# Performance work log

Hardware: AMD Instinct MI355X
Metric: run time of the kernel (lower is better)

Reference implementation:

```python
import jax, jax.numpy as jnp
import numpy as np

B, S, D, H = 16, 577, 1408, 16
HD = D // H  # 88


def setup_inputs() -> dict:
    key = jax.random.key(0)
    k1, k2, k3, k4, k5, k6 = jax.random.split(key, 6)
    hidden_states = jax.random.normal(k1, (B, S, D), dtype=jnp.float32)
    # realistic rotary table: cos/sin pairs stacked in last dim
    theta = jax.random.normal(k2, (S, HD // 2), dtype=jnp.float32)
    freqs_ci = jnp.stack([jnp.cos(theta), jnp.sin(theta)], axis=-1)  # (S, HD/2, 2)
    wqkv = jax.random.normal(k3, (3 * D, D), dtype=jnp.float32) * 0.02
    bqkv = jax.random.normal(k4, (3 * D,), dtype=jnp.float32) * 0.02
    wo = jax.random.normal(k5, (D, D), dtype=jnp.float32) * 0.02
    bo = jax.random.normal(k6, (D,), dtype=jnp.float32) * 0.02
    return {"hidden_states": hidden_states, "freqs_ci": freqs_ci,
            "wqkv": wqkv, "bqkv": bqkv, "wo": wo, "bo": bo}


def reference(hidden_states, freqs_ci, wqkv, bqkv, wo, bo):
    b, s, d = hidden_states.shape
    # fused QKV projection (torch Linear: x @ W.T + b)
    qkv = hidden_states @ wqkv.T + bqkv  # (B, S, 3D)
    q, k, v = jnp.split(qkv, 3, axis=-1)
    q = q.reshape(b, s, H, HD)
    k = k.reshape(b, s, H, HD)
    v = v.reshape(b, s, H, HD)

    cos = freqs_ci[..., 0][None, :, None, :]  # (1, S, 1, HD/2)
    sin = freqs_ci[..., 1][None, :, None, :]

    def rot(x):
        xr = x.reshape(b, s, H, HD // 2, 2)
        xe, xo = xr[..., 0], xr[..., 1]
        re = xe * cos - xo * sin
        ro = xe * sin + xo * cos
        return jnp.stack([re, ro], axis=-1).reshape(b, s, H, HD)

    q = rot(q)
    k = rot(k)

    scale = 1.0 / jnp.sqrt(jnp.float32(HD))  # SDPA default scaling
    scores = jnp.einsum('bqhd,bkhd->bhqk', q, k) * scale
    attn = jax.nn.softmax(scores, axis=-1)
    ctx = jnp.einsum('bhqk,bkhd->bqhd', attn, v).reshape(b, s, d)
    return ctx @ wo.T + bo
```

## Files before the change

kernel.cpp:

```cpp
#include <hip/hip_runtime.h>

typedef __attribute__((ext_vector_type(8))) __bf16 bf16x8;
typedef __attribute__((ext_vector_type(4))) float f32x4;
typedef __attribute__((ext_vector_type(4))) unsigned int uint4v;

#define B_ 16
#define S_ 577
#define D_ 1408
#define H_ 16
#define HD_ 88
#define MROWS (B_*S_)
#define N1 (3*D_)
#define K_ D_
#define KSTEPS 44
#define VT_LD 592
#define SCALE 0.10660035817780521f

static __device__ __forceinline__ void async16(void* lds, const void* g) {
  __builtin_amdgcn_global_load_lds((const __attribute__((address_space(1))) void*)g,
                                   (__attribute__((address_space(3))) void*)lds, 16, 0, 0);
}

static __device__ __forceinline__ int xcd_swizzle(int orig, int nwg) {
  int xcd = orig & 7, lid = orig >> 3;
  int q = nwg >> 3, r = nwg & 7;
  return (xcd < r ? xcd * (q + 1) : r * (q + 1) + (xcd - r) * q) + lid;
}

__global__ void cast_bf16_kernel(const float* __restrict__ src, __bf16* __restrict__ dst, int n4) {
  int i = blockIdx.x * blockDim.x + threadIdx.x;
  if (i >= n4) return;
  const float4 v = ((const float4*)src)[i];
  __bf16* d = dst + (size_t)i * 4;
  d[0] = (__bf16)v.x; d[1] = (__bf16)v.y; d[2] = (__bf16)v.z; d[3] = (__bf16)v.w;
}

__launch_bounds__(256, 2)
__global__ void gemm_qkv_rope(const __bf16* __restrict__ A, const __bf16* __restrict__ Bm,
                              const float* __restrict__ bias, const float* __restrict__ freqs,
                              __bf16* __restrict__ Qb, __bf16* __restrict__ Kb,
                              __bf16* __restrict__ Vb) {
  __shared__ __bf16 As[2][128 * 32];
  __shared__ __bf16 Bs[2][128 * 32];
  const int tid = threadIdx.x;
  const int w = tid >> 6, l = tid & 63;
  const int wgid = xcd_swizzle(blockIdx.x, 33 * 73);
  const int m0 = (wgid % 73) * 128, n0 = (wgid / 73) * 128;
  const int wr = w & 1, wc = w >> 1;
  const int M = MROWS, K = K_;

  f32x4 acc[4][4];
#pragma unroll
  for (int m = 0; m < 4; ++m)
#pragma unroll
    for (int n = 0; n < 4; ++n) acc[m][n] = (f32x4){0.f, 0.f, 0.f, 0.f};

  int arow0 = m0 + w * 32 + (l >> 2);      if (arow0 >= M) arow0 = M - 1;
  int arow1 = m0 + w * 32 + 16 + (l >> 2); if (arow1 >= M) arow1 = M - 1;
  const __bf16* ag0 = A + (size_t)arow0 * K + (l & 3) * 8;
  const __bf16* ag1 = A + (size_t)arow1 * K + (l & 3) * 8;
  const __bf16* bg0 = Bm + (size_t)(n0 + w * 32 + (l >> 2)) * K + (l & 3) * 8;
  const __bf16* bg1 = Bm + (size_t)(n0 + w * 32 + 16 + (l >> 2)) * K + (l & 3) * 8;

  auto stage = [&](int buf, int k0) {
    async16(&As[buf][(w * 32) * 32],      ag0 + k0);
    async16(&As[buf][(w * 32 + 16) * 32], ag1 + k0);
    async16(&Bs[buf][(w * 32) * 32],      bg0 + k0);
    async16(&Bs[buf][(w * 32 + 16) * 32], bg1 + k0);
  };

  stage(0, 0);
  __syncthreads();
  for (int t = 0; t < KSTEPS; ++t) {
    const int cur = t & 1;
    if (t < KSTEPS - 1) stage(cur ^ 1, (t + 1) * 32);
    bf16x8 a[4], b[4];
#pragma unroll
    for (int m = 0; m < 4; ++m)
      a[m] = *(const bf16x8*)&As[cur][(wr * 64 + m * 16 + (l & 15)) * 32 + (l >> 4) * 8];
#pragma unroll
    for (int n = 0; n < 4; ++n)
      b[n] = *(const bf16x8*)&Bs[cur][(wc * 64 + n * 16 + (l & 15)) * 32 + (l >> 4) * 8];
#pragma unroll
    for (int m = 0; m < 4; ++m)
#pragma unroll
      for (int n = 0; n < 4; ++n)
        acc[m][n] = __builtin_amdgcn_mfma_f32_16x16x32_bf16(a[m], b[n], acc[m][n], 0, 0, 0);
    __syncthreads();
  }

  const int sect = n0 / 1408;
  __bf16* dst = (sect == 0) ? Qb : (sect == 1 ? Kb : Vb);
#pragma unroll
  for (int n = 0; n < 4; ++n) {
    const int col = n0 + wc * 64 + n * 16 + (l & 15);
    const int cin = col - sect * 1408;
    const int h = cin / 88, d = cin % 88;
    const float bv = bias[col];
    const int i2 = d & ~1;
    const float sgn = (d & 1) ? 1.f : -1.f;
#pragma unroll
    for (int m = 0; m < 4; ++m) {
      const int rbase = m0 + wr * 64 + m * 16 + (l >> 4) * 4;
#pragma unroll
      for (int j = 0; j < 4; ++j) {
        const int r = rbase + j;
        float val = acc[m][n][j] + bv;
        const int s = r % 577;
        float outv;
        if (sect < 2) {
          const float2 cs = *(const float2*)&freqs[s * 88 + i2];
          const float p = __shfl_xor(val, 1);
          outv = val * cs.x + sgn * p * cs.y;
        } else {
          outv = val;
        }
        if (r < M) {
          const int b = r / 577;
          dst[((size_t)(b * 16 + h) * 577 + s) * 88 + d] = (__bf16)outv;
        }
      }
    }
  }
}

__launch_bounds__(256, 2)
__global__ void gemm_out_bias(const __bf16* __restrict__ A, const __bf16* __restrict__ Bm,
                              const float* __restrict__ bias, float* __restrict__ C) {
  __shared__ __bf16 As[2][128 * 32];
  __shared__ __bf16 Bs[2][128 * 32];
  const int tid = threadIdx.x;
  const int w = tid >> 6, l = tid & 63;
  const int wgid = xcd_swizzle(blockIdx.x, 11 * 73);
  const int m0 = (wgid % 73) * 128, n0 = (wgid / 73) * 128;
  const int wr = w & 1, wc = w >> 1;
  const int M = MROWS, N = D_, K = K_;

  f32x4 acc[4][4];
#pragma unroll
  for (int m = 0; m < 4; ++m)
#pragma unroll
    for (int n = 0; n < 4; ++n) acc[m][n] = (f32x4){0.f, 0.f, 0.f, 0.f};

  int arow0 = m0 + w * 32 + (l >> 2);      if (arow0 >= M) arow0 = M - 1;
  int arow1 = m0 + w * 32 + 16 + (l >> 2); if (arow1 >= M) arow1 = M - 1;
  const __bf16* ag0 = A + (size_t)arow0 * K + (l & 3) * 8;
  const __bf16* ag1 = A + (size_t)arow1 * K + (l & 3) * 8;
  const __bf16* bg0 = Bm + (size_t)(n0 + w * 32 + (l >> 2)) * K + (l & 3) * 8;
  const __bf16* bg1 = Bm + (size_t)(n0 + w * 32 + 16 + (l >> 2)) * K + (l & 3) * 8;

  auto stage = [&](int buf, int k0) {
    async16(&As[buf][(w * 32) * 32],      ag0 + k0);
    async16(&As[buf][(w * 32 + 16) * 32], ag1 + k0);
    async16(&Bs[buf][(w * 32) * 32],      bg0 + k0);
    async16(&Bs[buf][(w * 32 + 16) * 32], bg1 + k0);
  };

  stage(0, 0);
  __syncthreads();
  for (int t = 0; t < KSTEPS; ++t) {
    const int cur = t & 1;
    if (t < KSTEPS - 1) stage(cur ^ 1, (t + 1) * 32);
    bf16x8 a[4], b[4];
#pragma unroll
    for (int m = 0; m < 4; ++m)
      a[m] = *(const bf16x8*)&As[cur][(wr * 64 + m * 16 + (l & 15)) * 32 + (l >> 4) * 8];
#pragma unroll
    for (int n = 0; n < 4; ++n)
      b[n] = *(const bf16x8*)&Bs[cur][(wc * 64 + n * 16 + (l & 15)) * 32 + (l >> 4) * 8];
#pragma unroll
    for (int m = 0; m < 4; ++m)
#pragma unroll
      for (int n = 0; n < 4; ++n)
        acc[m][n] = __builtin_amdgcn_mfma_f32_16x16x32_bf16(a[m], b[n], acc[m][n], 0, 0, 0);
    __syncthreads();
  }

#pragma unroll
  for (int n = 0; n < 4; ++n) {
    int col = n0 + wc * 64 + n * 16 + (l & 15);
    float bv = bias[col];
#pragma unroll
    for (int m = 0; m < 4; ++m) {
      int rbase = m0 + wr * 64 + m * 16 + (l >> 4) * 4;
#pragma unroll
      for (int j = 0; j < 4; ++j) {
        int r = rbase + j;
        if (r < M) C[(size_t)r * N + col] = acc[m][n][j] + bv;
      }
    }
  }
}

__global__ void transpose_v(const __bf16* __restrict__ V, __bf16* __restrict__ Vt_g) {
  __shared__ __bf16 Ls[64 * 104];
  const int bh = blockIdx.x, t = blockIdx.y, s0 = t * 64;
  const int tid = threadIdx.x;
  const __bf16* vp = V + (size_t)bh * 577 * 88;
  for (int i = tid; i < 64 * 11; i += 256) {
    int r = i / 11, off = i % 11;
    int gs = s0 + r; if (gs > 576) gs = 576;
    *(uint4v*)&Ls[r * 104 + off * 8] = *(const uint4v*)(vp + (size_t)gs * 88 + off * 8);
  }
  __syncthreads();
  for (int i = tid; i < 88 * 8; i += 256) {
    int d = i / 8, so = (i % 8) * 8;
    int sc_ = s0 + so;
    if (sc_ < VT_LD) {
      __bf16 tmp[8];
#pragma unroll
      for (int j = 0; j < 8; ++j) tmp[j] = Ls[(so + j) * 104 + d];
      *(uint4v*)&Vt_g[((size_t)bh * 88 + d) * VT_LD + sc_] = *(uint4v*)tmp;
    }
  }
}

__launch_bounds__(256, 3)
__global__ void attn_kernel(const __bf16* __restrict__ Q, const __bf16* __restrict__ K,
                            const __bf16* __restrict__ Vt_gp, __bf16* __restrict__ ctx) {
  __shared__ __bf16 lds[26368];
  const int tid = threadIdx.x;
  const int w = tid >> 6, l = tid & 63;
  const int bh = blockIdx.x;
  const int q0 = blockIdx.y * 128;
  const __bf16* qp = Q + (size_t)bh * 577 * 88;
  const __bf16* kp = K + (size_t)bh * 577 * 88;
  const __bf16* vtp = Vt_gp + (size_t)bh * 88 * VT_LD;
  __bf16* Qs = lds;
  __bf16* Ks = lds + 12288;
  __bf16* Vt = lds + 17920;
  __bf16* Pw = lds + w * 2304;

  for (int i = tid; i < 128 * 11; i += 256) {
    int r = i / 11, off = i % 11;
    int gr = q0 + r; if (gr > 576) gr = 576;
    *(uint4v*)&Qs[r * 96 + off * 8] = *(const uint4v*)(qp + (size_t)gr * 88 + off * 8);
  }
  if (tid < 128) { uint4v z = 0; *(uint4v*)&Qs[tid * 96 + 88] = z; }
  __syncthreads();

  bf16x8 qf[2][3];
#pragma unroll
  for (int mg = 0; mg < 2; ++mg)
#pragma unroll
    for (int kk = 0; kk < 3; ++kk)
      qf[mg][kk] = *(const bf16x8*)&Qs[(w * 32 + mg * 16 + (l & 15)) * 96 + kk * 32 + (l >> 4) * 8];

  int preA[7], preB[7];
#pragma unroll
  for (int kch = 0; kch < 7; ++kch) {
    int c = w + 4 * kch;
    int a = 0, b2 = 0;
    if (c < 11) a = c * 512 + l * 8;
    else if (c < 27) { int e = (c - 11) * 512 + l * 8; a = (e / 88) * VT_LD; b2 = e % 88; }
    preA[kch] = a; preB[kch] = b2;
  }

  f32x4 oacc[2][6];
#pragma unroll
  for (int mg = 0; mg < 2; ++mg)
#pragma unroll
    for (int dn = 0; dn < 6; ++dn) oacc[mg][dn] = (f32x4){0.f, 0.f, 0.f, 0.f};
  f32x4 mrun[2], lrun[2];
  mrun[0] = -1e30f; mrun[1] = -1e30f;
  lrun[0] = 0.f; lrun[1] = 0.f;

  for (int t = 0; t < 10; ++t) {
    const int s0 = t * 64;
    if (t) __syncthreads();
#pragma unroll
    for (int kch = 0; kch < 7; ++kch) {
      int c = w + 4 * kch;
      if (c < 11) {
        async16(Ks + c * 512, kp + (size_t)s0 * 88 + preA[kch]);
      } else if (c < 27) {
        int g = s0 + preB[kch]; if (g > 584) g = 584;
        async16(Vt + (c - 11) * 512, vtp + preA[kch] + g);
      }
    }
    __syncthreads();

    f32x4 sc[2][4];
#pragma unroll
    for (int mg = 0; mg < 2; ++mg)
#pragma unroll
      for (int n = 0; n < 4; ++n) sc[mg][n] = (f32x4){0.f, 0.f, 0.f, 0.f};
#pragma unroll
    for (int n = 0; n < 4; ++n) {
#pragma unroll
      for (int kk = 0; kk < 3; ++kk) {
        bf16x8 kf = *(const bf16x8*)&Ks[(n * 16 + (l & 15)) * 88 + kk * 32 + (l >> 4) * 8];
        sc[0][n] = __builtin_amdgcn_mfma_f32_16x16x32_bf16(qf[0][kk], kf, sc[0][n], 0, 0, 0);
        sc[1][n] = __builtin_amdgcn_mfma_f32_16x16x32_bf16(qf[1][kk], kf, sc[1][n], 0, 0, 0);
      }
    }

    f32x4 tmax[2];
    tmax[0] = -1e30f; tmax[1] = -1e30f;
#pragma unroll
    for (int n = 0; n < 4; ++n) {
      const int kc = s0 + n * 16 + (l & 15);
      const bool valid = kc < 577;
#pragma unroll
      for (int mg = 0; mg < 2; ++mg)
#pragma unroll
        for (int j = 0; j < 4; ++j) {
          float v = valid ? sc[mg][n][j] * SCALE : -1e30f;
          sc[mg][n][j] = v;
          tmax[mg][j] = fmaxf(tmax[mg][j], v);
        }
    }
#pragma unroll
    for (int o = 1; o < 16; o <<= 1)
#pragma unroll
      for (int mg = 0; mg < 2; ++mg)
#pragma unroll
        for (int j = 0; j < 4; ++j)
          tmax[mg][j] = fmaxf(tmax[mg][j], __shfl_xor(tmax[mg][j], o));
#pragma unroll
    for (int mg = 0; mg < 2; ++mg)
#pragma unroll
      for (int j = 0; j < 4; ++j) {
        float mo = mrun[mg][j];
        float mn = fmaxf(mo, tmax[mg][j]);
        float sf = __expf(mo - mn);
        mrun[mg][j] = mn;
        lrun[mg][j] *= sf;
#pragma unroll
        for (int dn = 0; dn < 6; ++dn) oacc[mg][dn][j] *= sf;
      }
#pragma unroll
    for (int mg = 0; mg < 2; ++mg)
#pragma unroll
      for (int n = 0; n < 4; ++n)
#pragma unroll
        for (int j = 0; j < 4; ++j) {
          float p = __expf(sc[mg][n][j] - mrun[mg][j]);
          lrun[mg][j] += p;
          Pw[(mg * 16 + (l >> 4) * 4 + j) * 72 + n * 16 + (l & 15)] = (__bf16)p;
        }

#pragma unroll
    for (int ks = 0; ks < 2; ++ks) {
      bf16x8 pa0 = *(const bf16x8*)&Pw[((l & 15)) * 72 + ks * 32 + (l >> 4) * 8];
      bf16x8 pa1 = *(const bf16x8*)&Pw[(16 + (l & 15)) * 72 + ks * 32 + (l >> 4) * 8];
#pragma unroll
      for (int dn = 0; dn < 6; ++dn) {
        bf16x8 vb = *(const bf16x8*)&Vt[(dn * 16 + (l & 15)) * 88 + ks * 32 + (l >> 4) * 8];
        oacc[0][dn] = __builtin_amdgcn_mfma_f32_16x16x32_bf16(pa0, vb, oacc[0][dn], 0, 0, 0);
        oacc[1][dn] = __builtin_amdgcn_mfma_f32_16x16x32_bf16(pa1, vb, oacc[1][dn], 0, 0, 0);
      }
    }
  }

#pragma unroll
  for (int o = 1; o < 16; o <<= 1)
#pragma unroll
    for (int mg = 0; mg < 2; ++mg)
#pragma unroll
      for (int j = 0; j < 4; ++j)
        lrun[mg][j] += __shfl_xor(lrun[mg][j], o);

  const int b = bh >> 4, h = bh & 15;
#pragma unroll
  for (int mg = 0; mg < 2; ++mg) {
    float inv[4];
#pragma unroll
    for (int j = 0; j < 4; ++j) inv[j] = 1.f / lrun[mg][j];
    const int sqb = q0 + w * 32 + mg * 16 + (l >> 4) * 4;
#pragma unroll
    for (int dn = 0; dn < 6; ++dn) {
      const int d = dn * 16 + (l & 15);
      if (d >= 88) continue;
#pragma unroll
      for (int j = 0; j < 4; ++j) {
        const int sq = sqb + j;
        if (sq < 577)
          ctx[((size_t)(b * 577 + sq)) * 1408 + h * 88 + d] = (__bf16)(oacc[mg][dn][j] * inv[j]);
      }
    }
  }
}

extern "C" void kernel_launch(void* const* d_in, const int* in_sizes, int n_in,
                              void* d_out, int out_size, void* d_ws, size_t ws_size,
                              hipStream_t stream) {
  const float* hs    = (const float*)d_in[0];
  const float* freqs = (const float*)d_in[1];
  const float* wqkv  = (const float*)d_in[2];
  const float* bqkv  = (const float*)d_in[3];
  const float* wo    = (const float*)d_in[4];
  const float* bo    = (const float*)d_in[5];
  float* out = (float*)d_out;

  char* ws = (char*)d_ws;
  size_t off = 0;
  auto alloc = [&](size_t bytes) {
    void* p = ws + off;
    off += (bytes + 255) & ~(size_t)255;
    return p;
  };
  __bf16* x_bf    = (__bf16*)alloc((size_t)MROWS * K_ * 2);
  __bf16* ctx_bf  = x_bf;
  __bf16* wqkv_bf = (__bf16*)alloc((size_t)N1 * K_ * 2);
  __bf16* wo_bf   = (__bf16*)alloc((size_t)D_ * K_ * 2);
  __bf16* q_bf    = (__bf16*)alloc((size_t)MROWS * D_ * 2);
  __bf16* k_bf    = (__bf16*)alloc((size_t)MROWS * D_ * 2);
  __bf16* v_bf    = (__bf16*)alloc((size_t)MROWS * D_ * 2);
  __bf16* vt_g    = (__bf16*)d_out;

  cast_bf16_kernel<<<(MROWS * K_ / 4 + 255) / 256, 256, 0, stream>>>(hs, x_bf, MROWS * K_ / 4);
  cast_bf16_kernel<<<(N1 * K_ / 4 + 255) / 256, 256, 0, stream>>>(wqkv, wqkv_bf, N1 * K_ / 4);
  cast_bf16_kernel<<<(D_ * K_ / 4 + 255) / 256, 256, 0, stream>>>(wo, wo_bf, D_ * K_ / 4);

  gemm_qkv_rope<<<33 * 73, 256, 0, stream>>>(x_bf, wqkv_bf, bqkv, freqs, q_bf, k_bf, v_bf);

  transpose_v<<<dim3(256, 10), 256, 0, stream>>>(v_bf, vt_g);

  attn_kernel<<<dim3(256, 5), 256, 0, stream>>>(q_bf, k_bf, vt_g, ctx_bf);

  gemm_out_bias<<<11 * 73, 256, 0, stream>>>(ctx_bf, wo_bf, bo, out);
}
```

Before: 426.5 us.

## Rewrite both GEMMs with 256x256 tiles, swizzled LDS and ping-pong schedule

Both the QKV and output projection GEMMs now share a 512-thread core that computes 256x256 output tiles with K steps of 64. It uses XOR-swizzled LDS, double-buffered async global-to-LDS loads, and an interleaved read/MFMA schedule with explicit barriers and priority hints. The larger tiles raise data reuse per load and cut the number of workgroups. The cost is 128KB of LDS per block, which limits occupancy, plus wasted work on partial N tiles (4224 and 1408 are not multiples of 256).

```diff
diff --git a/kernel.cpp b/kernel.cpp
--- a/kernel.cpp
+++ b/kernel.cpp
@@ -12,7 +12,6 @@
 #define MROWS (B_*S_)
 #define N1 (3*D_)
 #define K_ D_
-#define KSTEPS 44
 #define VT_LD 592
 #define SCALE 0.10660035817780521f
 
@@ -26,6 +25,11 @@
   int q = nwg >> 3, r = nwg & 7;
   return (xcd < r ? xcd * (q + 1) : r * (q + 1) + (xcd - r) * q) + lid;
 }
+
+#define LGKM0() do { asm volatile("s_waitcnt lgkmcnt(0)" ::: "memory"); \
+                     __builtin_amdgcn_sched_barrier(0); } while (0)
+#define VMDRAIN() asm volatile("s_waitcnt vmcnt(0)" ::: "memory")
+#define BARR() __builtin_amdgcn_s_barrier()
 
 __global__ void cast_bf16_kernel(const float* __restrict__ src, __bf16* __restrict__ dst, int n4) {
   int i = blockIdx.x * blockDim.x + threadIdx.x;
@@ -35,87 +39,154 @@
   d[0] = (__bf16)v.x; d[1] = (__bf16)v.y; d[2] = (__bf16)v.z; d[3] = (__bf16)v.w;
 }
 
-__launch_bounds__(256, 2)
+__device__ __forceinline__ void gemm256_core(const __bf16* __restrict__ A,
+                                             const __bf16* __restrict__ Bm,
+                                             int m0, int n0, int Arows, int Brows,
+                                             __bf16* lds, f32x4 (&acc)[8][4]) {
+  const int tid = threadIdx.x;
+  const int w = tid >> 6, l = tid & 63;
+  const int wm = w >> 2, wn = w & 3;
+  const int l15 = l & 15;
+  const int x0 = (((l >> 4) * 8)) ^ ((l & 7) << 3);
+  const int x1 = ((32 + (l >> 4) * 8)) ^ ((l & 7) << 3);
+  const int sbase = w * 512;
+
+  const int lr = w * 8 + (l >> 3);
+  const int swc = ((l & 7) ^ (l >> 3)) * 8;
+  const __bf16* pa[2][2];
+  const __bf16* pb[2][2];
+#pragma unroll
+  for (int h = 0; h < 2; ++h)
+#pragma unroll
+    for (int r8 = 0; r8 < 2; ++r8) {
+      int ra = m0 + h * 128 + r8 * 64 + lr; if (ra >= Arows) ra = Arows - 1;
+      int rb = n0 + h * 128 + r8 * 64 + lr; if (rb >= Brows) rb = Brows - 1;
+      pa[h][r8] = A + (size_t)ra * K_ + swc;
+      pb[h][r8] = Bm + (size_t)rb * K_ + swc;
+    }
+
+#pragma unroll
+  for (int m = 0; m < 8; ++m)
+#pragma unroll
+    for (int n = 0; n < 4; ++n) acc[m][n] = (f32x4){0.f, 0.f, 0.f, 0.f};
+
+#pragma unroll
+  for (int h = 0; h < 2; ++h)
+#pragma unroll
+    for (int r8 = 0; r8 < 2; ++r8) {
+      async16(lds + h * 8192 + r8 * 4096 + sbase, pa[h][r8]);
+      async16(lds + 16384 + h * 8192 + r8 * 4096 + sbase, pb[h][r8]);
+    }
+  VMDRAIN();
+  BARR();
+
+  bf16x8 af[4][2], bfr[2][2];
+
+#define RD_A(MH) { _Pragma("unroll") for (int i = 0; i < 4; ++i) { \
+    const __bf16* rp = At + (wm * 128 + (MH) * 64 + i * 16 + l15) * 64; \
+    af[i][0] = *(const bf16x8*)(rp + x0); af[i][1] = *(const bf16x8*)(rp + x1); } }
+#define RD_B(NH) { _Pragma("unroll") for (int jn = 0; jn < 2; ++jn) { \
+    const __bf16* rp = Bt + (wn * 64 + (NH) * 32 + jn * 16 + l15) * 64; \
+    bfr[jn][0] = *(const bf16x8*)(rp + x0); bfr[jn][1] = *(const bf16x8*)(rp + x1); } }
+#define MM(MH, NH) { __builtin_amdgcn_s_setprio(1); \
+    _Pragma("unroll") for (int i = 0; i < 4; ++i) _Pragma("unroll") for (int jn = 0; jn < 2; ++jn) { \
+      acc[(MH)*4+i][(NH)*2+jn] = __builtin_amdgcn_mfma_f32_16x16x32_bf16(af[i][0], bfr[jn][0], acc[(MH)*4+i][(NH)*2+jn], 0, 0, 0); \
+      acc[(MH)*4+i][(NH)*2+jn] = __builtin_amdgcn_mfma_f32_16x16x32_bf16(af[i][1], bfr[jn][1], acc[(MH)*4+i][(NH)*2+jn], 0, 0, 0); } \
+    __builtin_amdgcn_s_setprio(0); }
+#define STG(WHICH, PP, KC) { _Pragma("unroll") for (int h = 0; h < 2; ++h) \
+    _Pragma("unroll") for (int r8 = 0; r8 < 2; ++r8) \
+      async16(Sd + (WHICH) * 16384 + h * 8192 + r8 * 4096 + sbase, PP[h][r8] + (KC)); }
+
+  for (int kt = 0; kt < 21; ++kt) {
+    __bf16* At = lds + (kt & 1) * 32768;
+    __bf16* Bt = At + 16384;
+    __bf16* Sd = lds + ((kt & 1) ^ 1) * 32768;
+    const int kc = (kt + 1) * 64;
+    RD_A(0); RD_B(0);
+    STG(0, pa, kc);
+    BARR(); LGKM0();
+    MM(0, 0);
+    BARR();
+    RD_A(1);
+    STG(1, pb, kc);
+    BARR(); LGKM0();
+    MM(1, 0);
+    BARR();
+    RD_B(1);
+    BARR(); LGKM0();
+    MM(1, 1);
+    BARR();
+    RD_A(0);
+    BARR(); LGKM0();
+    MM(0, 1);
+    VMDRAIN();
+    BARR();
+  }
+  {
+    __bf16* At = lds + 32768;
+    __bf16* Bt = At + 16384;
+    RD_A(0); RD_B(0);
+    BARR(); LGKM0();
+    MM(0, 0);
+    BARR();
+    RD_A(1);
+    BARR(); LGKM0();
+    MM(1, 0);
+    BARR();
+    RD_B(1);
+    BARR(); LGKM0();
+    MM(1, 1);
+    BARR();
+    RD_A(0);
+    BARR(); LGKM0();
+    MM(0, 1);
+  }
+#undef RD_A
+#undef RD_B
+#undef MM
+#undef STG
+}
+
+__launch_bounds__(512, 2)
 __global__ void gemm_qkv_rope(const __bf16* __restrict__ A, const __bf16* __restrict__ Bm,
                               const float* __restrict__ bias, const float* __restrict__ freqs,
                               __bf16* __restrict__ Qb, __bf16* __restrict__ Kb,
                               __bf16* __restrict__ Vb) {
-  __shared__ __bf16 As[2][128 * 32];
-  __shared__ __bf16 Bs[2][128 * 32];
+  __shared__ __align__(16) __bf16 lds[65536];
+  const int wgid = xcd_swizzle(blockIdx.x, 37 * 17);
+  const int m0 = (wgid % 37) * 256, n0 = (wgid / 37) * 256;
+  f32x4 acc[8][4];
+  gemm256_core(A, Bm, m0, n0, MROWS, N1, lds, acc);
+
   const int tid = threadIdx.x;
   const int w = tid >> 6, l = tid & 63;
-  const int wgid = xcd_swizzle(blockIdx.x, 33 * 73);
-  const int m0 = (wgid % 73) * 128, n0 = (wgid / 73) * 128;
-  const int wr = w & 1, wc = w >> 1;
-  const int M = MROWS, K = K_;
-
-  f32x4 acc[4][4];
-#pragma unroll
-  for (int m = 0; m < 4; ++m)
-#pragma unroll
-    for (int n = 0; n < 4; ++n) acc[m][n] = (f32x4){0.f, 0.f, 0.f, 0.f};
-
-  int arow0 = m0 + w * 32 + (l >> 2);      if (arow0 >= M) arow0 = M - 1;
-  int arow1 = m0 + w * 32 + 16 + (l >> 2); if (arow1 >= M) arow1 = M - 1;
-  const __bf16* ag0 = A + (size_t)arow0 * K + (l & 3) * 8;
-  const __bf16* ag1 = A + (size_t)arow1 * K + (l & 3) * 8;
-  const __bf16* bg0 = Bm + (size_t)(n0 + w * 32 + (l >> 2)) * K + (l & 3) * 8;
-  const __bf16* bg1 = Bm + (size_t)(n0 + w * 32 + 16 + (l >> 2)) * K + (l & 3) * 8;
-
-  auto stage = [&](int buf, int k0) {
-    async16(&As[buf][(w * 32) * 32],      ag0 + k0);
-    async16(&As[buf][(w * 32 + 16) * 32], ag1 + k0);
-    async16(&Bs[buf][(w * 32) * 32],      bg0 + k0);
-    async16(&Bs[buf][(w * 32 + 16) * 32], bg1 + k0);
-  };
-
-  stage(0, 0);
-  __syncthreads();
-  for (int t = 0; t < KSTEPS; ++t) {
-    const int cur = t & 1;
-    if (t < KSTEPS - 1) stage(cur ^ 1, (t + 1) * 32);
-    bf16x8 a[4], b[4];
-#pragma unroll
-    for (int m = 0; m < 4; ++m)
-      a[m] = *(const bf16x8*)&As[cur][(wr * 64 + m * 16 + (l & 15)) * 32 + (l >> 4) * 8];
-#pragma unroll
-    for (int n = 0; n < 4; ++n)
-      b[n] = *(const bf16x8*)&Bs[cur][(wc * 64 + n * 16 + (l & 15)) * 32 + (l >> 4) * 8];
-#pragma unroll
-    for (int m = 0; m < 4; ++m)
-#pragma unroll
-      for (int n = 0; n < 4; ++n)
-        acc[m][n] = __builtin_amdgcn_mfma_f32_16x16x32_bf16(a[m], b[n], acc[m][n], 0, 0, 0);
-    __syncthreads();
-  }
-
-  const int sect = n0 / 1408;
-  __bf16* dst = (sect == 0) ? Qb : (sect == 1 ? Kb : Vb);
+  const int wm = w >> 2, wn = w & 3;
 #pragma unroll
   for (int n = 0; n < 4; ++n) {
-    const int col = n0 + wc * 64 + n * 16 + (l & 15);
+    const int col = n0 + wn * 64 + n * 16 + (l & 15);
+    if (col >= N1) continue;
+    const int sect = col / 1408;
     const int cin = col - sect * 1408;
-    const int h = cin / 88, d = cin % 88;
+    const int h = cin / 88, d = cin - h * 88;
     const float bv = bias[col];
+    const float sgn = (d & 1) ? 1.f : -1.f;
     const int i2 = d & ~1;
-    const float sgn = (d & 1) ? 1.f : -1.f;
-#pragma unroll
-    for (int m = 0; m < 4; ++m) {
-      const int rbase = m0 + wr * 64 + m * 16 + (l >> 4) * 4;
+    __bf16* dst = (sect == 0) ? Qb : (sect == 1 ? Kb : Vb);
+#pragma unroll
+    for (int m = 0; m < 8; ++m) {
+      const int rb = m0 + wm * 128 + m * 16 + (l >> 4) * 4;
 #pragma unroll
       for (int j = 0; j < 4; ++j) {
-        const int r = rbase + j;
+        const int r = rb + j;
         float val = acc[m][n][j] + bv;
         const int s = r % 577;
-        float outv;
+        float outv = val;
         if (sect < 2) {
           const float2 cs = *(const float2*)&freqs[s * 88 + i2];
           const float p = __shfl_xor(val, 1);
           outv = val * cs.x + sgn * p * cs.y;
-        } else {
-          outv = val;
         }
-        if (r < M) {
+        if (r < MROWS) {
           const int b = r / 577;
           dst[((size_t)(b * 16 + h) * 577 + s) * 88 + d] = (__bf16)outv;
         }
@@ -124,69 +195,30 @@
   }
 }
 
-__launch_bounds__(256, 2)
+__launch_bounds__(512, 2)
 __global__ void gemm_out_bias(const __bf16* __restrict__ A, const __bf16* __restrict__ Bm,
                               const float* __restrict__ bias, float* __restrict__ C) {
-  __shared__ __bf16 As[2][128 * 32];
-  __shared__ __bf16 Bs[2][128 * 32];
+  __shared__ __align__(16) __bf16 lds[65536];
+  const int wgid = xcd_swizzle(blockIdx.x, 37 * 6);
+  const int m0 = (wgid % 37) * 256, n0 = (wgid / 37) * 256;
+  f32x4 acc[8][4];
+  gemm256_core(A, Bm, m0, n0, MROWS, D_, lds, acc);
+
   const int tid = threadIdx.x;
   const int w = tid >> 6, l = tid & 63;
-  const int wgid = xcd_swizzle(blockIdx.x, 11 * 73);
-  const int m0 = (wgid % 73) * 128, n0 = (wgid / 73) * 128;
-  const int wr = w & 1, wc = w >> 1;
-  const int M = MROWS, N = D_, K = K_;
-
-  f32x4 acc[4][4];
-#pragma unroll
-  for (int m = 0; m < 4; ++m)
-#pragma unroll
-    for (int n = 0; n < 4; ++n) acc[m][n] = (f32x4){0.f, 0.f, 0.f, 0.f};
-
-  int arow0 = m0 + w * 32 + (l >> 2);      if (arow0 >= M) arow0 = M - 1;
-  int arow1 = m0 + w * 32 + 16 + (l >> 2); if (arow1 >= M) arow1 = M - 1;
-  const __bf16* ag0 = A + (size_t)arow0 * K + (l & 3) * 8;
-  const __bf16* ag1 = A + (size_t)arow1 * K + (l & 3) * 8;
-  const __bf16* bg0 = Bm + (size_t)(n0 + w * 32 + (l >> 2)) * K + (l & 3) * 8;
-  const __bf16* bg1 = Bm + (size_t)(n0 + w * 32 + 16 + (l >> 2)) * K + (l & 3) * 8;
-
-  auto stage = [&](int buf, int k0) {
-    async16(&As[buf][(w * 32) * 32],      ag0 + k0);
-    async16(&As[buf][(w * 32 + 16) * 32], ag1 + k0);
-    async16(&Bs[buf][(w * 32) * 32],      bg0 + k0);
-    async16(&Bs[buf][(w * 32 + 16) * 32], bg1 + k0);
-  };
-
-  stage(0, 0);
-  __syncthreads();
-  for (int t = 0; t < KSTEPS; ++t) {
-    const int cur = t & 1;
-    if (t < KSTEPS - 1) stage(cur ^ 1, (t + 1) * 32);
-    bf16x8 a[4], b[4];
-#pragma unroll
-    for (int m = 0; m < 4; ++m)
-      a[m] = *(const bf16x8*)&As[cur][(wr * 64 + m * 16 + (l & 15)) * 32 + (l >> 4) * 8];
-#pragma unroll
-    for (int n = 0; n < 4; ++n)
-      b[n] = *(const bf16x8*)&Bs[cur][(wc * 64 + n * 16 + (l & 15)) * 32 + (l >> 4) * 8];
-#pragma unroll
-    for (int m = 0; m < 4; ++m)
-#pragma unroll
-      for (int n = 0; n < 4; ++n)
-        acc[m][n] = __builtin_amdgcn_mfma_f32_16x16x32_bf16(a[m], b[n], acc[m][n], 0, 0, 0);
-    __syncthreads();
-  }
-
+  const int wm = w >> 2, wn = w & 3;
 #pragma unroll
   for (int n = 0; n < 4; ++n) {
-    int col = n0 + wc * 64 + n * 16 + (l & 15);
-    float bv = bias[col];
-#pragma unroll
-    for (int m = 0; m < 4; ++m) {
-      int rbase = m0 + wr * 64 + m * 16 + (l >> 4) * 4;
+    const int col = n0 + wn * 64 + n * 16 + (l & 15);
+    if (col >= D_) continue;
+    const float bv = bias[col];
+#pragma unroll
+    for (int m = 0; m < 8; ++m) {
+      const int rb = m0 + wm * 128 + m * 16 + (l >> 4) * 4;
 #pragma unroll
       for (int j = 0; j < 4; ++j) {
-        int r = rbase + j;
-        if (r < M) C[(size_t)r * N + col] = acc[m][n][j] + bv;
+        const int r = rb + j;
+        if (r < MROWS) C[(size_t)r * D_ + col] = acc[m][n][j] + bv;
       }
     }
   }
@@ -413,11 +445,11 @@
   cast_bf16_kernel<<<(N1 * K_ / 4 + 255) / 256, 256, 0, stream>>>(wqkv, wqkv_bf, N1 * K_ / 4);
   cast_bf16_kernel<<<(D_ * K_ / 4 + 255) / 256, 256, 0, stream>>>(wo, wo_bf, D_ * K_ / 4);
 
-  gemm_qkv_rope<<<33 * 73, 256, 0, stream>>>(x_bf, wqkv_bf, bqkv, freqs, q_bf, k_bf, v_bf);
+  gemm_qkv_rope<<<37 * 17, 512, 0, stream>>>(x_bf, wqkv_bf, bqkv, freqs, q_bf, k_bf, v_bf);
 
   transpose_v<<<dim3(256, 10), 256, 0, stream>>>(v_bf, vt_g);
 
   attn_kernel<<<dim3(256, 5), 256, 0, stream>>>(q_bf, k_bf, vt_g, ctx_bf);
 
-  gemm_out_bias<<<11 * 73, 256, 0, stream>>>(ctx_bf, wo_bf, bo, out);
-}
+  gemm_out_bias<<<37 * 6, 512, 0, stream>>>(ctx_bf, wo_bf, bo, out);
+}
```

Measured after the change: 422.9 us. Within noise of the previous version (-0.9%).
